# Performance work log

Measured on AMD Instinct MI355X. Metric: run time of the kernel, lower is better.

Reference implementation:

```python
import jax, jax.numpy as jnp
import numpy as np

NUM_FIELDS = 50
CARD = 10000  # per-field cardinality; global index = x + field_offset
FACTOR_DIM = 64
ATT_SIZE = 64
BATCH = 2048


def setup_inputs() -> dict:
    key = jax.random.key(0)
    ks = jax.random.split(key, 5)
    x = jax.random.randint(ks[0], (BATCH, NUM_FIELDS), 0, CARD, dtype=jnp.int64)
    emb = jax.random.normal(ks[1], (NUM_FIELDS * CARD, FACTOR_DIM), jnp.float32) * 0.1
    W1 = jax.random.normal(ks[2], (FACTOR_DIM, ATT_SIZE), jnp.float32) * 0.1
    b1 = jnp.zeros((ATT_SIZE,), jnp.float32)
    w2 = jax.random.normal(ks[3], (ATT_SIZE, 1), jnp.float32) * 0.1
    b2 = jnp.zeros((1,), jnp.float32)
    lin_w = jax.random.normal(ks[4], (NUM_FIELDS * CARD, 1), jnp.float32) * 0.1
    lin_b = jnp.zeros((1,), jnp.float32)
    return {"x": x, "emb": emb, "W1": W1, "b1": b1, "w2": w2, "b2": b2,
            "lin_w": lin_w, "lin_b": lin_b}


def reference(x, emb, W1, b1, w2, b2, lin_w, lin_b):
    F = NUM_FIELDS
    offsets = (jnp.arange(F, dtype=x.dtype) * CARD)[None, :]  # [1, F]
    idx = x + offsets                                          # [B, F] global ids
    factors = emb[idx]                                         # [B, F, D]
    iu, ju = np.triu_indices(F, k=1)                           # P = F*(F-1)/2 pairs (i < j)
    inter = factors[:, iu, :] * factors[:, ju, :]              # [B, P, D]
    # attention MLP: Dense -> ReLU -> Dense(1) -> Softmax over pair axis
    h = jax.nn.relu(jnp.einsum('bpd,da->bpa', inter, W1) + b1)
    logits = jnp.einsum('bpa,ao->bpo', h, w2) + b2             # [B, P, 1]
    scores = jax.nn.softmax(logits, axis=1)
    inter_sum = jnp.sum(inter, axis=-1, keepdims=True)         # [B, P, 1]
    attended = jnp.sum(inter_sum * scores, axis=1)             # [B, 1]
    linear = jnp.sum(lin_w[idx], axis=1) + lin_b               # [B, 1]
    return linear + attended
```

## Files before the change

kernel.cpp:

```cpp
#include <hip/hip_runtime.h>
#include <hip/hip_bf16.h>

#define NF 50
#define NFP 52
#define NG 13
#define NCARD 10000
#define FD 64
#define FROW 72

typedef _Float16 h16x8 __attribute__((ext_vector_type(8)));
typedef float f32x4 __attribute__((ext_vector_type(4)));

__global__ void afm_pre(const float* __restrict__ W1, _Float16* __restrict__ w1f) {
    const int slot = blockIdx.x * 4 + (threadIdx.x >> 6);
    const int lane = threadIdx.x & 63;
    const int n16 = lane & 15, quad = lane >> 4;
    const int mt = slot >> 1, ks = slot & 1;
    h16x8 v;
    #pragma unroll
    for (int jj = 0; jj < 8; ++jj)
        v[jj] = (_Float16)W1[(ks * 32 + quad * 8 + jj) * 64 + mt * 16 + n16];
    *(h16x8*)(w1f + ((size_t)(slot * 64 + lane)) * 8) = v;
}

__global__ __launch_bounds__(256, 4) void afm_main(
    const int* __restrict__ x,
    const float* __restrict__ emb,
    const float* __restrict__ b1,
    const float* __restrict__ w2,
    const float* __restrict__ lin_w,
    const float* __restrict__ lin_b,
    const _Float16* __restrict__ w1f,
    float* __restrict__ out)
{
    __shared__ __align__(16) _Float16 fach[NFP * FROW];
    __shared__ float cmb[4][2];
    __shared__ float s_lin;

    const int b    = blockIdx.x;
    const int tid  = threadIdx.x;
    const int lane = tid & 63;
    const int wid  = tid >> 6;
    const int n16  = lane & 15;
    const int quad = lane >> 4;

    float linv = 0.f;
    if (wid == 3 && lane < NF)
        linv = lin_w[x[b * NF + lane] + lane * NCARD];

    for (int t = tid; t < NFP * 8; t += 256) {
        int f = t >> 3, q = t & 7;
        h16x8 h = {0, 0, 0, 0, 0, 0, 0, 0};
        if (f < NF) {
            int gid = x[b * NF + f] + f * NCARD;
            const float* src = emb + (size_t)gid * FD + q * 8;
            float4 v0 = *(const float4*)(src);
            float4 v1 = *(const float4*)(src + 4);
            h[0] = (_Float16)v0.x; h[1] = (_Float16)v0.y;
            h[2] = (_Float16)v0.z; h[3] = (_Float16)v0.w;
            h[4] = (_Float16)v1.x; h[5] = (_Float16)v1.y;
            h[6] = (_Float16)v1.z; h[7] = (_Float16)v1.w;
        }
        *(h16x8*)(fach + (size_t)f * FROW + q * 8) = h;
    }

    h16x8 afragW[8];
    #pragma unroll
    for (int s = 0; s < 8; ++s)
        afragW[s] = *(const h16x8*)(w1f + ((size_t)(s * 64 + lane)) * 8);
    h16x8 aones = {(_Float16)1, (_Float16)1, (_Float16)1, (_Float16)1,
                   (_Float16)1, (_Float16)1, (_Float16)1, (_Float16)1};
    f32x4 b1v[4], w2v[4];
    #pragma unroll
    for (int mt = 0; mt < 4; ++mt) {
        const float4 bb = *(const float4*)(b1 + mt * 16 + quad * 4);
        const float4 ww = *(const float4*)(w2 + mt * 16 + quad * 4);
        b1v[mt] = (f32x4){bb.x, bb.y, bb.z, bb.w};
        w2v[mt] = (f32x4){ww.x, ww.y, ww.z, ww.w};
    }
    __syncthreads();

    const int a4 = n16 >> 2, b4 = n16 & 3;
    float se = 0.f, sei = 0.f;

    for (int gi = wid; gi < NG; gi += 4) {
        const int i = gi * 4 + a4;
        const _Float16* ri = fach + (size_t)i * FROW + quad * 8;
        const h16x8 ri0 = *(const h16x8*)(ri);
        const h16x8 ri1 = *(const h16x8*)(ri + 32);

        const _Float16* rjp = fach + (size_t)(gi * 4 + b4) * FROW + quad * 8;
        h16x8 nj0 = *(const h16x8*)(rjp);
        h16x8 nj1 = *(const h16x8*)(rjp + 32);

        for (int gj = gi; gj < NG; ++gj) {
            h16x8 rj0 = nj0, rj1 = nj1;
            if (gj + 1 < NG) {
                rjp += 4 * FROW;
                nj0 = *(const h16x8*)(rjp);
                nj1 = *(const h16x8*)(rjp + 32);
            }
            h16x8 pr0 = ri0 * rj0;
            h16x8 pr1 = ri1 * rj1;

            f32x4 accS = __builtin_amdgcn_mfma_f32_16x16x32_f16(aones, pr0, (f32x4){0.f, 0.f, 0.f, 0.f}, 0, 0, 0);
            accS = __builtin_amdgcn_mfma_f32_16x16x32_f16(aones, pr1, accS, 0, 0, 0);

            float lp[4];
            #pragma unroll
            for (int mt = 0; mt < 4; ++mt) {
                f32x4 acc = __builtin_amdgcn_mfma_f32_16x16x32_f16(afragW[mt * 2 + 0], pr0, b1v[mt], 0, 0, 0);
                acc = __builtin_amdgcn_mfma_f32_16x16x32_f16(afragW[mt * 2 + 1], pr1, acc, 0, 0, 0);
                float s0 = fmaxf(acc[0], 0.f) * w2v[mt][0] + fmaxf(acc[1], 0.f) * w2v[mt][1];
                float s1 = fmaxf(acc[2], 0.f) * w2v[mt][2] + fmaxf(acc[3], 0.f) * w2v[mt][3];
                lp[mt] = s0 + s1;
            }
            float lacc = (lp[0] + lp[1]) + (lp[2] + lp[3]);
            lacc += __shfl_xor(lacc, 16, 64);
            lacc += __shfl_xor(lacc, 32, 64);

            const int j = gj * 4 + b4;
            const bool valid = (i < j) && (j < NF);
            float e = valid ? __expf(lacc) : 0.f;
            se  += e;
            sei += e * accS[0];
        }
    }

    #pragma unroll
    for (int d = 1; d <= 8; d <<= 1) {
        se  += __shfl_xor(se, d, 64);
        sei += __shfl_xor(sei, d, 64);
    }
    if (wid == 3) {
        #pragma unroll
        for (int d = 1; d <= 32; d <<= 1) linv += __shfl_xor(linv, d, 64);
        if (lane == 0) s_lin = linv;
    }
    if (lane == 0) { cmb[wid][0] = se; cmb[wid][1] = sei; }
    __syncthreads();
    if (tid == 0) {
        float tse  = (cmb[0][0] + cmb[1][0]) + (cmb[2][0] + cmb[3][0]);
        float tsei = (cmb[0][1] + cmb[1][1]) + (cmb[2][1] + cmb[3][1]);
        out[b] = s_lin + lin_b[0] + tsei / tse;
    }
}

extern "C" void kernel_launch(void* const* d_in, const int* in_sizes, int n_in,
                              void* d_out, int out_size, void* d_ws, size_t ws_size,
                              hipStream_t stream) {
    const int*   x     = (const int*)d_in[0];
    const float* emb   = (const float*)d_in[1];
    const float* W1    = (const float*)d_in[2];
    const float* b1    = (const float*)d_in[3];
    const float* w2    = (const float*)d_in[4];
    const float* lin_w = (const float*)d_in[6];
    const float* lin_b = (const float*)d_in[7];
    float* out = (float*)d_out;

    _Float16* w1f = (_Float16*)d_ws;
    afm_pre<<<2, 256, 0, stream>>>(W1, w1f);
    const int batch = out_size;
    afm_main<<<batch, 256, 0, stream>>>(x, emb, b1, w2, lin_w, lin_b, w1f, out);
}
```

Measured before the change: 216.6 us.

## Use one wavefront per batch row and fold W1 conversion into main kernel

Each block now holds a single 64-lane wavefront that processes every pair group for its batch row, instead of four waves splitting the groups and combining their sums through shared memory and a barrier. The separate W1 preprocessing kernel is removed, and each wave instead gathers and converts W1 to fp16 fragments directly from global memory. This cuts one kernel launch and the cross-wave reduction, but gives each block four times the serial work and adds 64 strided W1 loads per wave. Latency hiding must now come from having more resident blocks per CU.

```diff
diff --git a/kernel.cpp b/kernel.cpp
--- a/kernel.cpp
+++ b/kernel.cpp
@@ -11,44 +11,28 @@
 typedef _Float16 h16x8 __attribute__((ext_vector_type(8)));
 typedef float f32x4 __attribute__((ext_vector_type(4)));
 
-__global__ void afm_pre(const float* __restrict__ W1, _Float16* __restrict__ w1f) {
-    const int slot = blockIdx.x * 4 + (threadIdx.x >> 6);
-    const int lane = threadIdx.x & 63;
-    const int n16 = lane & 15, quad = lane >> 4;
-    const int mt = slot >> 1, ks = slot & 1;
-    h16x8 v;
-    #pragma unroll
-    for (int jj = 0; jj < 8; ++jj)
-        v[jj] = (_Float16)W1[(ks * 32 + quad * 8 + jj) * 64 + mt * 16 + n16];
-    *(h16x8*)(w1f + ((size_t)(slot * 64 + lane)) * 8) = v;
-}
-
-__global__ __launch_bounds__(256, 4) void afm_main(
+__global__ __launch_bounds__(64) void afm_main(
     const int* __restrict__ x,
     const float* __restrict__ emb,
+    const float* __restrict__ W1,
     const float* __restrict__ b1,
     const float* __restrict__ w2,
     const float* __restrict__ lin_w,
     const float* __restrict__ lin_b,
-    const _Float16* __restrict__ w1f,
     float* __restrict__ out)
 {
     __shared__ __align__(16) _Float16 fach[NFP * FROW];
-    __shared__ float cmb[4][2];
-    __shared__ float s_lin;
 
     const int b    = blockIdx.x;
-    const int tid  = threadIdx.x;
-    const int lane = tid & 63;
-    const int wid  = tid >> 6;
+    const int lane = threadIdx.x;
     const int n16  = lane & 15;
     const int quad = lane >> 4;
 
     float linv = 0.f;
-    if (wid == 3 && lane < NF)
+    if (lane < NF)
         linv = lin_w[x[b * NF + lane] + lane * NCARD];
 
-    for (int t = tid; t < NFP * 8; t += 256) {
+    for (int t = lane; t < NFP * 8; t += 64) {
         int f = t >> 3, q = t & 7;
         h16x8 h = {0, 0, 0, 0, 0, 0, 0, 0};
         if (f < NF) {
@@ -66,8 +50,15 @@
 
     h16x8 afragW[8];
     #pragma unroll
-    for (int s = 0; s < 8; ++s)
-        afragW[s] = *(const h16x8*)(w1f + ((size_t)(s * 64 + lane)) * 8);
+    for (int mt = 0; mt < 4; ++mt)
+        #pragma unroll
+        for (int ks = 0; ks < 2; ++ks) {
+            h16x8 v;
+            #pragma unroll
+            for (int jj = 0; jj < 8; ++jj)
+                v[jj] = (_Float16)W1[(ks * 32 + quad * 8 + jj) * 64 + mt * 16 + n16];
+            afragW[mt * 2 + ks] = v;
+        }
     h16x8 aones = {(_Float16)1, (_Float16)1, (_Float16)1, (_Float16)1,
                    (_Float16)1, (_Float16)1, (_Float16)1, (_Float16)1};
     f32x4 b1v[4], w2v[4];
@@ -83,7 +74,7 @@
     const int a4 = n16 >> 2, b4 = n16 & 3;
     float se = 0.f, sei = 0.f;
 
-    for (int gi = wid; gi < NG; gi += 4) {
+    for (int gi = 0; gi < NG; ++gi) {
         const int i = gi * 4 + a4;
         const _Float16* ri = fach + (size_t)i * FROW + quad * 8;
         const h16x8 ri0 = *(const h16x8*)(ri);
@@ -132,18 +123,11 @@
         se  += __shfl_xor(se, d, 64);
         sei += __shfl_xor(sei, d, 64);
     }
-    if (wid == 3) {
-        #pragma unroll
-        for (int d = 1; d <= 32; d <<= 1) linv += __shfl_xor(linv, d, 64);
-        if (lane == 0) s_lin = linv;
-    }
-    if (lane == 0) { cmb[wid][0] = se; cmb[wid][1] = sei; }
-    __syncthreads();
-    if (tid == 0) {
-        float tse  = (cmb[0][0] + cmb[1][0]) + (cmb[2][0] + cmb[3][0]);
-        float tsei = (cmb[0][1] + cmb[1][1]) + (cmb[2][1] + cmb[3][1]);
-        out[b] = s_lin + lin_b[0] + tsei / tse;
-    }
+    #pragma unroll
+    for (int d = 1; d <= 32; d <<= 1) linv += __shfl_xor(linv, d, 64);
+
+    if (lane == 0)
+        out[b] = linv + lin_b[0] + sei / se;
 }
 
 extern "C" void kernel_launch(void* const* d_in, const int* in_sizes, int n_in,
@@ -157,9 +141,6 @@
     const float* lin_w = (const float*)d_in[6];
     const float* lin_b = (const float*)d_in[7];
     float* out = (float*)d_out;
-
-    _Float16* w1f = (_Float16*)d_ws;
-    afm_pre<<<2, 256, 0, stream>>>(W1, w1f);
     const int batch = out_size;
-    afm_main<<<batch, 256, 0, stream>>>(x, emb, b1, w2, lin_w, lin_b, w1f, out);
+    afm_main<<<batch, 64, 0, stream>>>(x, emb, W1, b1, w2, lin_w, lin_b, out);
 }
```

Result: slower. 221.7 us (+2.4%).
